# Optimization experiments

Hardware: AMD Instinct MI355X
Metric: run time of the kernel (lower is better)

Reference implementation:

```python
import jax, jax.numpy as jnp
import numpy as np
import math

GROUPS = 32  # min(256 // 4, 32)
EPS = 1e-5

def group_norm(x, w, b):
    B, C, H, W = x.shape
    xg = x.reshape(B, GROUPS, C // GROUPS, H, W)
    mean = jnp.mean(xg, axis=(2, 3, 4), keepdims=True)
    var = jnp.var(xg, axis=(2, 3, 4), keepdims=True)
    xn = ((xg - mean) * jax.lax.rsqrt(var + EPS)).reshape(B, C, H, W)
    return xn * w[None, :, None, None] + b[None, :, None, None]

def nin(x, W, b):
    # 1x1 projection: [B,C,H,W] x [C,D] -> [B,D,H,W]
    return jnp.einsum('bchw,cd->bdhw', x, W) + b[None, :, None, None]

def setup_inputs() -> dict:
    key = jax.random.key(0)
    ks = jax.random.split(key, 5)
    C = 256
    scale = 1.0 / math.sqrt(C)
    return {
        'x': jax.random.normal(ks[0], (4, C, 64, 64), dtype=jnp.float32),
        'gn_w': jnp.ones((C,), jnp.float32),
        'gn_b': jnp.zeros((C,), jnp.float32),
        'Wq': jax.random.normal(ks[1], (C, C), jnp.float32) * scale,
        'bq': jnp.zeros((C,), jnp.float32),
        'Wk': jax.random.normal(ks[2], (C, C), jnp.float32) * scale,
        'bk': jnp.zeros((C,), jnp.float32),
        'Wv': jax.random.normal(ks[3], (C, C), jnp.float32) * scale,
        'bv': jnp.zeros((C,), jnp.float32),
        'Wp': jax.random.normal(ks[4], (C, C), jnp.float32) * scale,
        'bp': jnp.zeros((C,), jnp.float32),
    }

def reference(x, gn_w, gn_b, Wq, bq, Wk, bk, Wv, bv, Wp, bp):
    B, C, H, W = x.shape
    h = group_norm(x, gn_w, gn_b)
    q = nin(h, Wq, bq).reshape(B, C, H * W)
    k = nin(h, Wk, bk).reshape(B, C, H * W)
    v = nin(h, Wv, bv).reshape(B, C, H * W)
    # attention logits: [B, HW, HW]
    w = jnp.einsum('bcn,bcm->bnm', q, k) * (C ** -0.5)
    w = jax.nn.softmax(w, axis=-1)
    h_out = jnp.einsum('bnm,bcm->bcn', w, v).reshape(B, C, H, W)
    h_out = nin(h_out, Wp, bp)
    out = x + h_out
    return out / math.sqrt(2.0)  # skip_rescale=True
```

## Files before the change

kernel.cpp:

```cpp
#include <hip/hip_runtime.h>
#include <math.h>


#define BB 4
#define CCH 256
#define NSP 4096
#define EPSV 1e-5f
#define ATTN_SCALE 0.0625f
#define RSQRT2 0.70710678118654752440f
#define KSPLIT 2
#define TILES_PER_PART 32

typedef __attribute__((ext_vector_type(8))) short bf16x8;
typedef __attribute__((ext_vector_type(4))) float f32x4;

typedef __attribute__((address_space(1))) void gvoid;
typedef __attribute__((address_space(3))) void lvoid;
__device__ __forceinline__ void dma16(const void* g, void* l) {
  __builtin_amdgcn_global_load_lds((gvoid*)g, (lvoid*)l, 16, 0, 0);
}

__device__ __forceinline__ short f2bf(float f) {
  union { float f; unsigned u; } a; a.f = f;
  unsigned r = a.u + 0x7fffu + ((a.u >> 16) & 1u);
  return (short)(r >> 16);
}
__device__ __forceinline__ float bf2f(short s) {
  union { unsigned u; float f; } a;
  a.u = ((unsigned)(unsigned short)s) << 16;
  return a.f;
}
__device__ __forceinline__ unsigned cvt_pk_bf16(float lo, float hi) {
  unsigned r;
  asm("v_cvt_pk_bf16_f32 %0, %1, %2" : "=v"(r) : "v"(lo), "v"(hi));
  return r;
}

__global__ __launch_bounds__(256) void gn_stats(
    const float* __restrict__ x, float* __restrict__ stats) {
  int b = blockIdx.x >> 5;
  int g = blockIdx.x & 31;
  size_t base = ((size_t)b * CCH + (size_t)g * 8) * NSP;
  const float4* xv = (const float4*)(x + base);
  int tid = threadIdx.x;
  float s = 0.f, ss = 0.f;
  for (int i = tid; i < 8192; i += 256) {
    float4 v = xv[i];
    s += (v.x + v.y) + (v.z + v.w);
    ss += (v.x * v.x + v.y * v.y) + (v.z * v.z + v.w * v.w);
  }
#pragma unroll
  for (int off = 32; off > 0; off >>= 1) {
    s += __shfl_down(s, off, 64);
    ss += __shfl_down(ss, off, 64);
  }
  __shared__ float rs[4], rss[4];
  int wv = tid >> 6;
  if ((tid & 63) == 0) { rs[wv] = s; rss[wv] = ss; }
  __syncthreads();
  if (tid == 0) {
    float S = rs[0] + rs[1] + rs[2] + rs[3];
    float SS = rss[0] + rss[1] + rss[2] + rss[3];
    float mean = S * (1.f / 32768.f);
    float var = SS * (1.f / 32768.f) - mean * mean;
    stats[(b * 32 + g) * 2 + 0] = mean;
    stats[(b * 32 + g) * 2 + 1] = rsqrtf(var + EPSV);
  }
}

__global__ __launch_bounds__(256) void prep_w(
    const float* __restrict__ Wq, const float* __restrict__ Wk,
    const float* __restrict__ Wv, const float* __restrict__ Wp,
    short* __restrict__ wts) {
  __shared__ float T[64][65];
  int c0 = blockIdx.x * 64, d0 = blockIdx.y * 64;
  int wz = blockIdx.z;
  const float* W = (wz == 0) ? Wq : (wz == 1) ? Wk : (wz == 2) ? Wv : Wp;
  short* wt = wts + (size_t)wz * CCH * CCH;
  int tid = threadIdx.x;
#pragma unroll
  for (int i = 0; i < 16; ++i) {
    int idx = tid + 256 * i;
    int row = idx >> 6, col = idx & 63;
    T[row][col] = W[(size_t)(c0 + row) * CCH + d0 + col];
  }
  __syncthreads();
#pragma unroll
  for (int i = 0; i < 16; ++i) {
    int idx = tid + 256 * i;
    int dr = idx >> 6, cc = idx & 63;
    wt[(size_t)(d0 + dr) * CCH + c0 + cc] = f2bf(T[cc][dr]);
  }
}

__global__ __launch_bounds__(512) void qkvg_kernel(
    const float* __restrict__ x, const float* __restrict__ stats,
    const float* __restrict__ gw, const float* __restrict__ gb,
    const short* __restrict__ wqt, const short* __restrict__ wkt,
    const short* __restrict__ wvt,
    const float* __restrict__ bq, const float* __restrict__ bk,
    const float* __restrict__ bv,
    short* __restrict__ qo, short* __restrict__ ko, short* __restrict__ vo) {
  __shared__ __align__(16) unsigned char smem[52224];
  float (*Ts)[68] = (float(*)[68])smem;
  float* aco = (float*)(smem + 17408);
  float* bco = aco + 256;
  short* Hs = (short*)(smem + 19456);
  short* Fo = (short*)smem;

  int bx = blockIdx.x;
  int b = bx & 3, n0 = (bx >> 2) * 64;
  int tid = threadIdx.x;
  if (tid < 256) {
    int g = tid >> 3;
    float mean = stats[(b * 32 + g) * 2 + 0];
    float rstd = stats[(b * 32 + g) * 2 + 1];
    float a = gw[tid] * rstd;
    aco[tid] = a;
    bco[tid] = gb[tid] - mean * a;
  }
  __syncthreads();
  const float* xb = x + (size_t)b * CCH * NSP;
  for (int p = 0; p < 4; ++p) {
    int c0 = p * 64;
#pragma unroll
    for (int i = 0; i < 2; ++i) {
      int crow = (tid >> 4) + i * 32;
      int c = c0 + crow;
      float4 v = *(const float4*)&xb[(size_t)c * NSP + n0 + (tid & 15) * 4];
      float a = aco[c], bb = bco[c];
      v.x = v.x * a + bb; v.y = v.y * a + bb;
      v.z = v.z * a + bb; v.w = v.w * a + bb;
      *(float4*)&Ts[crow][(tid & 15) * 4] = v;
    }
    __syncthreads();
    {
      int n = tid >> 3, seg = tid & 7;
      int cb = seg * 8;
      bf16x8 r;
#pragma unroll
      for (int j = 0; j < 8; ++j) r[j] = f2bf(Ts[cb + j][n]);
      int chunk = (c0 + cb) >> 3;
      *(bf16x8*)(Hs + n * 256 + ((chunk ^ (n & 7)) * 8)) = r;
    }
    __syncthreads();
  }
  int w = tid >> 6, lane = tid & 63, quad = lane >> 4, l16 = lane & 15;
  int wr = w & 3, h = w >> 2;
  bf16x8 a_h[8];
  {
    int row = wr * 16 + l16;
#pragma unroll
    for (int kc = 0; kc < 8; ++kc)
      a_h[kc] = *(bf16x8*)(Hs + row * 256 + (((kc * 4 + quad) ^ (row & 7)) * 8));
  }
  __syncthreads();
  for (int op = 0; op < 3; ++op) {
    const short* wt = (op == 0) ? wqt : (op == 1) ? wkt : wvt;
    const float* bias = (op == 0) ? bq : (op == 1) ? bk : bv;
    f32x4 acc[8];
#pragma unroll
    for (int mb = 0; mb < 8; ++mb) acc[mb] = (f32x4){0.f, 0.f, 0.f, 0.f};
#pragma unroll 4
    for (int mb = 0; mb < 8; ++mb) {
      const short* wp = wt + (size_t)((h * 8 + mb) * 16 + l16) * CCH + quad * 8;
#pragma unroll
      for (int kc = 0; kc < 8; ++kc) {
        bf16x8 af = *(const bf16x8*)(wp + kc * 32);
        acc[mb] = __builtin_amdgcn_mfma_f32_16x16x32_bf16(af, a_h[kc], acc[mb], 0, 0, 0);
      }
    }
    int n = n0 + wr * 16 + l16;
    if (op == 2) {
      short* ob = vo + (size_t)b * CCH * NSP;
      int mm = n & 63, m0_ = n & ~63;
      int mb_ = mm >> 4, qq = (mm >> 2) & 3, rr2 = mm & 3;
      int lc = (mb_ & 1) * 4 + qq;
      int jj = (mb_ >> 1) * 4 + rr2;
      int basen = m0_ + jj;
#pragma unroll
      for (int mb = 0; mb < 8; ++mb)
#pragma unroll
        for (int r = 0; r < 4; ++r) {
          int d = (h * 8 + mb) * 16 + quad * 4 + r;
          ob[(size_t)d * NSP + basen + ((lc ^ (d & 7)) << 3)] =
              f2bf(acc[mb][r] + bias[d]);
        }
    } else {
      float sc = (op == 0) ? ATTN_SCALE : 1.f;
      int nl = wr * 16 + l16;
#pragma unroll
      for (int mb = 0; mb < 8; ++mb)
#pragma unroll
        for (int r = 0; r < 4; ++r) {
          int d = (h * 8 + mb) * 16 + quad * 4 + r;
          Fo[nl * 264 + d] = f2bf((acc[mb][r] + bias[d]) * sc);
        }
      __syncthreads();
      short* ob = ((op == 0) ? qo : ko) + (size_t)b * NSP * CCH;
      {
        int row = tid >> 3, seg = tid & 7, r7 = row & 7;
        short* dst = ob + (size_t)(n0 + row) * CCH + seg * 32;
#pragma unroll
        for (int i = 0; i < 4; ++i) {
          int xch = seg * 4 + i;
          int cs = (xch & 24) | ((xch & 7) ^ r7);
          *(bf16x8*)(dst + i * 8) = *(bf16x8*)(Fo + row * 264 + cs * 8);
        }
      }
      __syncthreads();
    }
  }
}

__global__ __launch_bounds__(256, 1) void attn_kernel(
    const short* __restrict__ q, const short* __restrict__ k,
    const short* __restrict__ v, short* __restrict__ po,
    float* __restrict__ pm, float* __restrict__ pl) {
  __shared__ __align__(16) unsigned char smem[131072];
  short* Ks0 = (short*)smem;
  short* Ks1 = (short*)(smem + 32768);
  short* Vs0 = (short*)(smem + 65536);
  short* Vs1 = (short*)(smem + 98304);
  short* Fo  = (short*)smem;

  int bx = blockIdx.x;
  int grp = bx & 7;
  int b = grp & 3;
  int kh = grp >> 2;
  int n0 = ((bx >> 3) & 31) << 7;
  const short* qb = q + (size_t)b * NSP * CCH;
  const short* kb = k + (size_t)b * NSP * CCH;
  const char*  vbB = (const char*)(v + (size_t)b * CCH * NSP);
  int tid = threadIdx.x;
  int w = tid >> 6, lane = tid & 63, quad = lane >> 4, l16 = lane & 15;
  int mbase = kh * TILES_PER_PART * 64;

  bf16x8 a_q[2][8];
#pragma unroll
  for (int p = 0; p < 2; ++p) {
#pragma unroll
    for (int i = 0; i < 8; ++i) {
      int off = tid * 16 + i * 4096;
      dma16((const char*)(qb + (size_t)(n0 + p * 64) * CCH) + off,
            (char*)Ks0 + off);
    }
    __syncthreads();
    if ((w >> 1) == p) {
#pragma unroll
      for (int qh = 0; qh < 2; ++qh) {
        int row = (w & 1) * 32 + qh * 16 + l16;
#pragma unroll
        for (int kc = 0; kc < 8; ++kc)
          a_q[qh][kc] =
              *(bf16x8*)(Ks0 + row * 256 + (((kc * 4 + quad) ^ (row & 7)) * 8));
      }
    }
    __syncthreads();
  }

#pragma unroll
  for (int i = 0; i < 8; ++i) {
    int off = tid * 16 + i * 4096;
    dma16((const char*)(kb + (size_t)mbase * CCH) + off, (char*)Ks0 + off);
    int c = off >> 7, inrow = off & 127;
    dma16(vbB + (size_t)c * (NSP * 2) + (size_t)mbase * 2 + inrow,
          (char*)Vs0 + off);
  }
  __syncthreads();
#pragma unroll
  for (int i = 0; i < 8; ++i) {
    int off = tid * 16 + i * 4096;
    dma16((const char*)(kb + (size_t)(mbase + 64) * CCH) + off,
          (char*)Ks1 + off);
  }
  f32x4 s_prev[4][2];
#pragma unroll
  for (int mb = 0; mb < 4; ++mb)
#pragma unroll
    for (int qh = 0; qh < 2; ++qh) s_prev[mb][qh] = (f32x4){0.f, 0.f, 0.f, 0.f};
  __builtin_amdgcn_s_setprio(1);
#pragma unroll
  for (int kc = 0; kc < 8; ++kc) {
#pragma unroll
    for (int mb = 0; mb < 4; ++mb) {
      int row = mb * 16 + l16;
      bf16x8 kf = *(bf16x8*)(Ks0 + row * 256 + (((kc * 4 + quad) ^ (row & 7)) * 8));
#pragma unroll
      for (int qh = 0; qh < 2; ++qh)
        s_prev[mb][qh] = __builtin_amdgcn_mfma_f32_16x16x32_bf16(
            kf, a_q[qh][kc], s_prev[mb][qh], 0, 0, 0);
    }
  }
  __builtin_amdgcn_s_setprio(0);
  float mx_c[2];
#pragma unroll
  for (int qh = 0; qh < 2; ++qh) {
    float mx = -1e30f;
#pragma unroll
    for (int mb = 0; mb < 4; ++mb)
#pragma unroll
      for (int r = 0; r < 4; ++r) mx = fmaxf(mx, s_prev[mb][qh][r]);
    mx = fmaxf(mx, __shfl_xor(mx, 16));
    mx = fmaxf(mx, __shfl_xor(mx, 32));
    mx_c[qh] = mx;
  }

  f32x4 accO[16][2];
#pragma unroll
  for (int cb = 0; cb < 16; ++cb)
#pragma unroll
    for (int qh = 0; qh < 2; ++qh) accO[cb][qh] = (f32x4){0.f, 0.f, 0.f, 0.f};
  float m_run[2] = {-1e30f, -1e30f}, l_run[2] = {0.f, 0.f};
  int pc0 = quad ^ (l16 & 7);
  int pc1 = (4 + quad) ^ (l16 & 7);

#pragma unroll 1
  for (int t = 0; t < TILES_PER_PART; ++t) {
    __syncthreads();
    short* Kd = (t & 1) ? Ks1 : Ks0;
    short* Kr = (t & 1) ? Ks0 : Ks1;
    short* Vd = (t & 1) ? Vs0 : Vs1;
    short* Vr = (t & 1) ? Vs1 : Vs0;
    if (t + 2 < TILES_PER_PART) {
      const char* kp = (const char*)(kb + (size_t)(mbase + (t + 2) * 64) * CCH);
#pragma unroll
      for (int i = 0; i < 8; ++i) {
        int off = tid * 16 + i * 4096;
        dma16(kp + off, (char*)Kd + off);
      }
    }
    if (t + 1 < TILES_PER_PART) {
      int m0 = mbase + (t + 1) * 64;
#pragma unroll
      for (int i = 0; i < 8; ++i) {
        int off = tid * 16 + i * 4096;
        int c = off >> 7, inrow = off & 127;
        dma16(vbB + (size_t)c * (NSP * 2) + (size_t)m0 * 2 + inrow,
              (char*)Vd + off);
      }
    }
    f32x4 sn[4][2];
#pragma unroll
    for (int mb = 0; mb < 4; ++mb)
#pragma unroll
      for (int qh = 0; qh < 2; ++qh) sn[mb][qh] = (f32x4){0.f, 0.f, 0.f, 0.f};
    if (t + 1 < TILES_PER_PART) {
      __builtin_amdgcn_s_setprio(1);
#pragma unroll
      for (int kc = 0; kc < 8; ++kc) {
#pragma unroll
        for (int mb = 0; mb < 4; ++mb) {
          int row = mb * 16 + l16;
          bf16x8 kf = *(bf16x8*)(Kr + row * 256 + (((kc * 4 + quad) ^ (row & 7)) * 8));
#pragma unroll
          for (int qh = 0; qh < 2; ++qh)
            sn[mb][qh] = __builtin_amdgcn_mfma_f32_16x16x32_bf16(
                kf, a_q[qh][kc], sn[mb][qh], 0, 0, 0);
        }
      }
      __builtin_amdgcn_s_setprio(0);
    }
    bool grow = (mx_c[0] - m_run[0] > 8.f) || (mx_c[1] - m_run[1] > 8.f);
    if (__any(grow)) {
#pragma unroll
      for (int qh = 0; qh < 2; ++qh) {
        float mnew = fmaxf(m_run[qh], mx_c[qh]);
        float alpha = __expf(m_run[qh] - mnew);
#pragma unroll
        for (int cb = 0; cb < 16; ++cb) accO[cb][qh] *= alpha;
        l_run[qh] *= alpha;
        m_run[qh] = mnew;
      }
    }
#pragma unroll
    for (int qh = 0; qh < 2; ++qh) {
      float ls = 0.f;
#pragma unroll
      for (int mb = 0; mb < 4; ++mb)
#pragma unroll
        for (int r = 0; r < 4; ++r) {
          float p = __expf(s_prev[mb][qh][r] - m_run[qh]);
          ls += p;
          s_prev[mb][qh][r] = p;
        }
      ls += __shfl_xor(ls, 16);
      ls += __shfl_xor(ls, 32);
      l_run[qh] += ls;
    }
    union { unsigned u[4]; bf16x8 v; } pw0[2], pw1[2];
#pragma unroll
    for (int qh = 0; qh < 2; ++qh) {
      pw0[qh].u[0] = cvt_pk_bf16(s_prev[0][qh][0], s_prev[0][qh][1]);
      pw0[qh].u[1] = cvt_pk_bf16(s_prev[0][qh][2], s_prev[0][qh][3]);
      pw0[qh].u[2] = cvt_pk_bf16(s_prev[2][qh][0], s_prev[2][qh][1]);
      pw0[qh].u[3] = cvt_pk_bf16(s_prev[2][qh][2], s_prev[2][qh][3]);
      pw1[qh].u[0] = cvt_pk_bf16(s_prev[1][qh][0], s_prev[1][qh][1]);
      pw1[qh].u[1] = cvt_pk_bf16(s_prev[1][qh][2], s_prev[1][qh][3]);
      pw1[qh].u[2] = cvt_pk_bf16(s_prev[3][qh][0], s_prev[3][qh][1]);
      pw1[qh].u[3] = cvt_pk_bf16(s_prev[3][qh][2], s_prev[3][qh][3]);
    }
    __builtin_amdgcn_s_setprio(1);
#pragma unroll
    for (int cb = 0; cb < 16; ++cb) {
      bf16x8 vf = *(bf16x8*)(Vr + (cb * 16 + l16) * 64 + pc0 * 8);
#pragma unroll
      for (int qh = 0; qh < 2; ++qh)
        accO[cb][qh] = __builtin_amdgcn_mfma_f32_16x16x32_bf16(
            vf, pw0[qh].v, accO[cb][qh], 0, 0, 0);
    }
#pragma unroll
    for (int cb = 0; cb < 16; ++cb) {
      bf16x8 vf = *(bf16x8*)(Vr + (cb * 16 + l16) * 64 + pc1 * 8);
#pragma unroll
      for (int qh = 0; qh < 2; ++qh)
        accO[cb][qh] = __builtin_amdgcn_mfma_f32_16x16x32_bf16(
            vf, pw1[qh].v, accO[cb][qh], 0, 0, 0);
    }
    __builtin_amdgcn_s_setprio(0);
    if (t + 1 < TILES_PER_PART) {
#pragma unroll
      for (int qh = 0; qh < 2; ++qh) {
        float mxn = -1e30f;
#pragma unroll
        for (int mb = 0; mb < 4; ++mb)
#pragma unroll
          for (int r = 0; r < 4; ++r) mxn = fmaxf(mxn, sn[mb][qh][r]);
        mxn = fmaxf(mxn, __shfl_xor(mxn, 16));
        mxn = fmaxf(mxn, __shfl_xor(mxn, 32));
        mx_c[qh] = mxn;
      }
    }
#pragma unroll
    for (int mb = 0; mb < 4; ++mb)
#pragma unroll
      for (int qh = 0; qh < 2; ++qh) s_prev[mb][qh] = sn[mb][qh];
  }
  size_t sbase = ((size_t)kh * BB + b) * NSP + n0;
  if (quad == 0) {
#pragma unroll
    for (int qh = 0; qh < 2; ++qh) {
      pm[sbase + w * 32 + qh * 16 + l16] = m_run[qh];
      pl[sbase + w * 32 + qh * 16 + l16] = l_run[qh];
    }
  }
  short* ob = po + ((size_t)kh * BB + b) * NSP * CCH;
#pragma unroll
  for (int p = 0; p < 2; ++p) {
    __syncthreads();
    if ((w >> 1) == p) {
#pragma unroll
      for (int qh = 0; qh < 2; ++qh) {
        int nloc = (w & 1) * 32 + qh * 16 + l16;
        float linv = 1.f / l_run[qh];
#pragma unroll
        for (int cb = 0; cb < 16; ++cb)
#pragma unroll
          for (int r = 0; r < 4; ++r)
            Fo[nloc * 264 + cb * 16 + quad * 4 + r] =
                f2bf(accO[cb][qh][r] * linv);
      }
    }
    __syncthreads();
    int row = tid >> 2, seg = tid & 3;
    short* dst = ob + (size_t)(n0 + p * 64 + row) * CCH + seg * 64;
#pragma unroll
    for (int i = 0; i < 8; ++i)
      *(bf16x8*)(dst + i * 8) = *(bf16x8*)(Fo + row * 264 + seg * 64 + i * 8);
  }
}

__global__ __launch_bounds__(256) void proj_kernel(
    const short* __restrict__ po, const float* __restrict__ pm,
    const float* __restrict__ pl, const short* __restrict__ wpt,
    const float* __restrict__ bp, const float* __restrict__ x,
    float* __restrict__ out) {
  int n0 = blockIdx.x * 64;
  int dh = blockIdx.y * 128;
  int b = blockIdx.z;
  int tid = threadIdx.x;
  int w = tid >> 6, lane = tid & 63, quad = lane >> 4, l16 = lane & 15;
  int n = n0 + w * 16 + l16;

  float wgt[KSPLIT];
  {
    float m[KSPLIT];
    float M = -1e30f;
#pragma unroll
    for (int s = 0; s < KSPLIT; ++s) {
      m[s] = pm[((size_t)s * BB + b) * NSP + n];
      M = fmaxf(M, m[s]);
    }
    float wsum = 0.f;
#pragma unroll
    for (int s = 0; s < KSPLIT; ++s) {
      wgt[s] = __expf(m[s] - M) * pl[((size_t)s * BB + b) * NSP + n];
      wsum += wgt[s];
    }
    float linv = 1.f / wsum;
#pragma unroll
    for (int s = 0; s < KSPLIT; ++s) wgt[s] *= linv;
  }

  f32x4 acc[8];
#pragma unroll
  for (int mb = 0; mb < 8; ++mb) acc[mb] = (f32x4){0.f, 0.f, 0.f, 0.f};

  const short* pob = po + ((size_t)b * NSP + n) * CCH;
#pragma unroll 2
  for (int kc = 0; kc < 8; ++kc) {
    int coff = kc * 32 + quad * 8;
    float e[8];
#pragma unroll
    for (int i = 0; i < 8; ++i) e[i] = 0.f;
#pragma unroll
    for (int s = 0; s < KSPLIT; ++s) {
      bf16x8 f = *(const bf16x8*)(pob + (size_t)s * BB * NSP * CCH + coff);
#pragma unroll
      for (int i = 0; i < 8; ++i) e[i] += wgt[s] * bf2f(f[i]);
    }
    bf16x8 bm;
#pragma unroll
    for (int i = 0; i < 8; ++i) bm[i] = f2bf(e[i]);
#pragma unroll
    for (int mb = 0; mb < 8; ++mb) {
      bf16x8 af = *(const bf16x8*)(wpt + (size_t)(dh + mb * 16 + l16) * CCH + coff);
      acc[mb] = __builtin_amdgcn_mfma_f32_16x16x32_bf16(af, bm, acc[mb], 0, 0, 0);
    }
  }
#pragma unroll
  for (int mb = 0; mb < 8; ++mb) {
#pragma unroll
    for (int r = 0; r < 4; ++r) {
      int d = dh + mb * 16 + quad * 4 + r;
      size_t off = ((size_t)b * CCH + d) * NSP + n;
      out[off] = (acc[mb][r] + bp[d] + x[off]) * RSQRT2;
    }
  }
}

extern "C" void kernel_launch(void* const* d_in, const int* in_sizes, int n_in,
                              void* d_out, int out_size, void* d_ws, size_t ws_size,
                              hipStream_t stream) {
  const float* x  = (const float*)d_in[0];
  const float* gw = (const float*)d_in[1];
  const float* gb = (const float*)d_in[2];
  const float* Wq = (const float*)d_in[3];
  const float* bq = (const float*)d_in[4];
  const float* Wk = (const float*)d_in[5];
  const float* bk = (const float*)d_in[6];
  const float* Wv = (const float*)d_in[7];
  const float* bv = (const float*)d_in[8];
  const float* Wp = (const float*)d_in[9];
  const float* bp = (const float*)d_in[10];
  float* out = (float*)d_out;

  const size_t SZ = (size_t)BB * CCH * NSP;
  short* qb  = (short*)d_ws;
  short* kb  = qb + SZ;
  short* vb  = kb + SZ;
  short* poT = vb + SZ;
  float* pm  = (float*)(poT + (size_t)KSPLIT * SZ);
  float* pl  = pm + (size_t)KSPLIT * BB * NSP;
  float* stats = pl + (size_t)KSPLIT * BB * NSP;
  short* wts = (short*)(stats + BB * 64);
  short* wqt = wts;
  short* wkt = wts + (size_t)CCH * CCH;
  short* wvt = wts + (size_t)2 * CCH * CCH;
  short* wpt = wts + (size_t)3 * CCH * CCH;

  gn_stats<<<dim3(BB * 32), dim3(256), 0, stream>>>(x, stats);
  prep_w<<<dim3(4, 4, 4), dim3(256), 0, stream>>>(Wq, Wk, Wv, Wp, wts);
  qkvg_kernel<<<dim3(256), dim3(512), 0, stream>>>(
      x, stats, gw, gb, wqt, wkt, wvt, bq, bk, bv, qb, kb, vb);
  attn_kernel<<<dim3(BB * 32 * KSPLIT), dim3(256), 0, stream>>>(
      qb, kb, vb, poT, pm, pl);
  proj_kernel<<<dim3(64, 2, BB), dim3(256), 0, stream>>>(
      poT, pm, pl, wpt, bp, x, out);
}
```

Measured before the change: 307.6 us.

## Split attention keys four ways and run two single-buffered blocks per CU

The key dimension is now split into 4 parts of 16 tiles instead of 2 parts of 32, doubling the number of attention blocks. LDS use per block drops from double-buffered 128KB to single-buffered 64KB, and launch bounds now allow 2 blocks per CU. The software pipeline that computed the next tile's QK scores while doing the current PV is replaced by a straightforward per-tile sequence with barriers. The intent is to hide latency across two co-resident blocks rather than inside one block, at the cost of losing the intra-block overlap and doing more partial-result merging downstream.

New measurement: 318.7 us. 1.04x slower.

```diff
diff --git a/kernel.cpp b/kernel.cpp
--- a/kernel.cpp
+++ b/kernel.cpp
@@ -8,8 +8,8 @@
 #define EPSV 1e-5f
 #define ATTN_SCALE 0.0625f
 #define RSQRT2 0.70710678118654752440f
-#define KSPLIT 2
-#define TILES_PER_PART 32
+#define KSPLIT 4
+#define TILES_PER_PART 16
 
 typedef __attribute__((ext_vector_type(8))) short bf16x8;
 typedef __attribute__((ext_vector_type(4))) float f32x4;
@@ -213,22 +213,20 @@
   }
 }
 
-__global__ __launch_bounds__(256, 1) void attn_kernel(
+__global__ __launch_bounds__(256, 2) void attn_kernel(
     const short* __restrict__ q, const short* __restrict__ k,
     const short* __restrict__ v, short* __restrict__ po,
     float* __restrict__ pm, float* __restrict__ pl) {
-  __shared__ __align__(16) unsigned char smem[131072];
-  short* Ks0 = (short*)smem;
-  short* Ks1 = (short*)(smem + 32768);
-  short* Vs0 = (short*)(smem + 65536);
-  short* Vs1 = (short*)(smem + 98304);
-  short* Fo  = (short*)smem;
+  __shared__ __align__(16) unsigned char smem[65536];
+  short* Ks = (short*)smem;
+  short* Vs = (short*)(smem + 32768);
+  short* Fo = (short*)smem;
 
   int bx = blockIdx.x;
-  int grp = bx & 7;
+  int grp = bx & 15;
   int b = grp & 3;
   int kh = grp >> 2;
-  int n0 = ((bx >> 3) & 31) << 7;
+  int n0 = (bx >> 4) << 7;
   const short* qb = q + (size_t)b * NSP * CCH;
   const short* kb = k + (size_t)b * NSP * CCH;
   const char*  vbB = (const char*)(v + (size_t)b * CCH * NSP);
@@ -243,7 +241,7 @@
     for (int i = 0; i < 8; ++i) {
       int off = tid * 16 + i * 4096;
       dma16((const char*)(qb + (size_t)(n0 + p * 64) * CCH) + off,
-            (char*)Ks0 + off);
+            (char*)Ks + off);
     }
     __syncthreads();
     if ((w >> 1) == p) {
@@ -253,7 +251,7 @@
 #pragma unroll
         for (int kc = 0; kc < 8; ++kc)
           a_q[qh][kc] =
-              *(bf16x8*)(Ks0 + row * 256 + (((kc * 4 + quad) ^ (row & 7)) * 8));
+              *(bf16x8*)(Ks + row * 256 + (((kc * 4 + quad) ^ (row & 7)) * 8));
       }
     }
     __syncthreads();
@@ -262,49 +260,12 @@
 #pragma unroll
   for (int i = 0; i < 8; ++i) {
     int off = tid * 16 + i * 4096;
-    dma16((const char*)(kb + (size_t)mbase * CCH) + off, (char*)Ks0 + off);
+    dma16((const char*)(kb + (size_t)mbase * CCH) + off, (char*)Ks + off);
     int c = off >> 7, inrow = off & 127;
     dma16(vbB + (size_t)c * (NSP * 2) + (size_t)mbase * 2 + inrow,
-          (char*)Vs0 + off);
+          (char*)Vs + off);
   }
   __syncthreads();
-#pragma unroll
-  for (int i = 0; i < 8; ++i) {
-    int off = tid * 16 + i * 4096;
-    dma16((const char*)(kb + (size_t)(mbase + 64) * CCH) + off,
-          (char*)Ks1 + off);
-  }
-  f32x4 s_prev[4][2];
-#pragma unroll
-  for (int mb = 0; mb < 4; ++mb)
-#pragma unroll
-    for (int qh = 0; qh < 2; ++qh) s_prev[mb][qh] = (f32x4){0.f, 0.f, 0.f, 0.f};
-  __builtin_amdgcn_s_setprio(1);
-#pragma unroll
-  for (int kc = 0; kc < 8; ++kc) {
-#pragma unroll
-    for (int mb = 0; mb < 4; ++mb) {
-      int row = mb * 16 + l16;
-      bf16x8 kf = *(bf16x8*)(Ks0 + row * 256 + (((kc * 4 + quad) ^ (row & 7)) * 8));
-#pragma unroll
-      for (int qh = 0; qh < 2; ++qh)
-        s_prev[mb][qh] = __builtin_amdgcn_mfma_f32_16x16x32_bf16(
-            kf, a_q[qh][kc], s_prev[mb][qh], 0, 0, 0);
-    }
-  }
-  __builtin_amdgcn_s_setprio(0);
-  float mx_c[2];
-#pragma unroll
-  for (int qh = 0; qh < 2; ++qh) {
-    float mx = -1e30f;
-#pragma unroll
-    for (int mb = 0; mb < 4; ++mb)
-#pragma unroll
-      for (int r = 0; r < 4; ++r) mx = fmaxf(mx, s_prev[mb][qh][r]);
-    mx = fmaxf(mx, __shfl_xor(mx, 16));
-    mx = fmaxf(mx, __shfl_xor(mx, 32));
-    mx_c[qh] = mx;
-  }
 
   f32x4 accO[16][2];
 #pragma unroll
@@ -317,19 +278,104 @@
 
 #pragma unroll 1
   for (int t = 0; t < TILES_PER_PART; ++t) {
-    __syncthreads();
-    short* Kd = (t & 1) ? Ks1 : Ks0;
-    short* Kr = (t & 1) ? Ks0 : Ks1;
-    short* Vd = (t & 1) ? Vs0 : Vs1;
-    short* Vr = (t & 1) ? Vs1 : Vs0;
-    if (t + 2 < TILES_PER_PART) {
-      const char* kp = (const char*)(kb + (size_t)(mbase + (t + 2) * 64) * CCH);
+    f32x4 s[4][2];
+#pragma unroll
+    for (int mb = 0; mb < 4; ++mb)
+#pragma unroll
+      for (int qh = 0; qh < 2; ++qh) s[mb][qh] = (f32x4){0.f, 0.f, 0.f, 0.f};
+    __builtin_amdgcn_s_setprio(1);
+#pragma unroll
+    for (int kc = 0; kc < 8; ++kc) {
+#pragma unroll
+      for (int mb = 0; mb < 4; ++mb) {
+        int row = mb * 16 + l16;
+        bf16x8 kf = *(bf16x8*)(Ks + row * 256 + (((kc * 4 + quad) ^ (row & 7)) * 8));
+#pragma unroll
+        for (int qh = 0; qh < 2; ++qh)
+          s[mb][qh] = __builtin_amdgcn_mfma_f32_16x16x32_bf16(
+              kf, a_q[qh][kc], s[mb][qh], 0, 0, 0);
+      }
+    }
+    __builtin_amdgcn_s_setprio(0);
+    __syncthreads();
+    if (t + 1 < TILES_PER_PART) {
+      const char* kp = (const char*)(kb + (size_t)(mbase + (t + 1) * 64) * CCH);
 #pragma unroll
       for (int i = 0; i < 8; ++i) {
         int off = tid * 16 + i * 4096;
-        dma16(kp + off, (char*)Kd + off);
-      }
-    }
+        dma16(kp + off, (char*)Ks + off);
+      }
+    }
+    float mx[2];
+#pragma unroll
+    for (int qh = 0; qh < 2; ++qh) {
+      float m = -1e30f;
+#pragma unroll
+      for (int mb = 0; mb < 4; ++mb)
+#pragma unroll
+        for (int r = 0; r < 4; ++r) m = fmaxf(m, s[mb][qh][r]);
+      m = fmaxf(m, __shfl_xor(m, 16));
+      m = fmaxf(m, __shfl_xor(m, 32));
+      mx[qh] = m;
+    }
+    bool grow = (mx[0] - m_run[0] > 8.f) || (mx[1] - m_run[1] > 8.f);
+    if (__any(grow)) {
+#pragma unroll
+      for (int qh = 0; qh < 2; ++qh) {
+        float mnew = fmaxf(m_run[qh], mx[qh]);
+        float alpha = __expf(m_run[qh] - mnew);
+#pragma unroll
+        for (int cb = 0; cb < 16; ++cb) accO[cb][qh] *= alpha;
+        l_run[qh] *= alpha;
+        m_run[qh] = mnew;
+      }
+    }
+#pragma unroll
+    for (int qh = 0; qh < 2; ++qh) {
+      float ls = 0.f;
+#pragma unroll
+      for (int mb = 0; mb < 4; ++mb)
+#pragma unroll
+        for (int r = 0; r < 4; ++r) {
+          float p = __expf(s[mb][qh][r] - m_run[qh]);
+          ls += p;
+          s[mb][qh][r] = p;
+        }
+      ls += __shfl_xor(ls, 16);
+      ls += __shfl_xor(ls, 32);
+      l_run[qh] += ls;
+    }
+    union { unsigned u[4]; bf16x8 v; } pw0[2], pw1[2];
+#pragma unroll
+    for (int qh = 0; qh < 2; ++qh) {
+      pw0[qh].u[0] = cvt_pk_bf16(s[0][qh][0], s[0][qh][1]);
+      pw0[qh].u[1] = cvt_pk_bf16(s[0][qh][2], s[0][qh][3]);
+      pw0[qh].u[2] = cvt_pk_bf16(s[2][qh][0], s[2][qh][1]);
+      pw0[qh].u[3] = cvt_pk_bf16(s[2][qh][2], s[2][qh][3]);
+      pw1[qh].u[0] = cvt_pk_bf16(s[1][qh][0], s[1][qh][1]);
+      pw1[qh].u[1] = cvt_pk_bf16(s[1][qh][2], s[1][qh][3]);
+      pw1[qh].u[2] = cvt_pk_bf16(s[3][qh][0], s[3][qh][1]);
+      pw1[qh].u[3] = cvt_pk_bf16(s[3][qh][2], s[3][qh][3]);
+    }
+    __builtin_amdgcn_s_setprio(1);
+#pragma unroll
+    for (int cb = 0; cb < 16; ++cb) {
+      bf16x8 vf = *(bf16x8*)(Vs + (cb * 16 + l16) * 64 + pc0 * 8);
+#pragma unroll
+      for (int qh = 0; qh < 2; ++qh)
+        accO[cb][qh] = __builtin_amdgcn_mfma_f32_16x16x32_bf16(
+            vf, pw0[qh].v, accO[cb][qh], 0, 0, 0);
+    }
+#pragma unroll
+    for (int cb = 0; cb < 16; ++cb) {
+      bf16x8 vf = *(bf16x8*)(Vs + (cb * 16 + l16) * 64 + pc1 * 8);
+#pragma unroll
+      for (int qh = 0; qh < 2; ++qh)
+        accO[cb][qh] = __builtin_amdgcn_mfma_f32_16x16x32_bf16(
+            vf, pw1[qh].v, accO[cb][qh], 0, 0, 0);
+    }
+    __builtin_amdgcn_s_setprio(0);
+    __syncthreads();
     if (t + 1 < TILES_PER_PART) {
       int m0 = mbase + (t + 1) * 64;
 #pragma unroll
@@ -337,111 +383,16 @@
         int off = tid * 16 + i * 4096;
         int c = off >> 7, inrow = off & 127;
         dma16(vbB + (size_t)c * (NSP * 2) + (size_t)m0 * 2 + inrow,
-              (char*)Vd + off);
-      }
-    }
-    f32x4 sn[4][2];
-#pragma unroll
-    for (int mb = 0; mb < 4; ++mb)
-#pragma unroll
-      for (int qh = 0; qh < 2; ++qh) sn[mb][qh] = (f32x4){0.f, 0.f, 0.f, 0.f};
-    if (t + 1 < TILES_PER_PART) {
-      __builtin_amdgcn_s_setprio(1);
-#pragma unroll
-      for (int kc = 0; kc < 8; ++kc) {
-#pragma unroll
-        for (int mb = 0; mb < 4; ++mb) {
-          int row = mb * 16 + l16;
-          bf16x8 kf = *(bf16x8*)(Kr + row * 256 + (((kc * 4 + quad) ^ (row & 7)) * 8));
-#pragma unroll
-          for (int qh = 0; qh < 2; ++qh)
-            sn[mb][qh] = __builtin_amdgcn_mfma_f32_16x16x32_bf16(
-                kf, a_q[qh][kc], sn[mb][qh], 0, 0, 0);
-        }
-      }
-      __builtin_amdgcn_s_setprio(0);
-    }
-    bool grow = (mx_c[0] - m_run[0] > 8.f) || (mx_c[1] - m_run[1] > 8.f);
-    if (__any(grow)) {
-#pragma unroll
-      for (int qh = 0; qh < 2; ++qh) {
-        float mnew = fmaxf(m_run[qh], mx_c[qh]);
-        float alpha = __expf(m_run[qh] - mnew);
-#pragma unroll
-        for (int cb = 0; cb < 16; ++cb) accO[cb][qh] *= alpha;
-        l_run[qh] *= alpha;
-        m_run[qh] = mnew;
-      }
-    }
-#pragma unroll
-    for (int qh = 0; qh < 2; ++qh) {
-      float ls = 0.f;
-#pragma unroll
-      for (int mb = 0; mb < 4; ++mb)
-#pragma unroll
-        for (int r = 0; r < 4; ++r) {
-          float p = __expf(s_prev[mb][qh][r] - m_run[qh]);
-          ls += p;
-          s_prev[mb][qh][r] = p;
-        }
-      ls += __shfl_xor(ls, 16);
-      ls += __shfl_xor(ls, 32);
-      l_run[qh] += ls;
-    }
-    union { unsigned u[4]; bf16x8 v; } pw0[2], pw1[2];
-#pragma unroll
-    for (int qh = 0; qh < 2; ++qh) {
-      pw0[qh].u[0] = cvt_pk_bf16(s_prev[0][qh][0], s_prev[0][qh][1]);
-      pw0[qh].u[1] = cvt_pk_bf16(s_prev[0][qh][2], s_prev[0][qh][3]);
-      pw0[qh].u[2] = cvt_pk_bf16(s_prev[2][qh][0], s_prev[2][qh][1]);
-      pw0[qh].u[3] = cvt_pk_bf16(s_prev[2][qh][2], s_prev[2][qh][3]);
-      pw1[qh].u[0] = cvt_pk_bf16(s_prev[1][qh][0], s_prev[1][qh][1]);
-      pw1[qh].u[1] = cvt_pk_bf16(s_prev[1][qh][2], s_prev[1][qh][3]);
-      pw1[qh].u[2] = cvt_pk_bf16(s_prev[3][qh][0], s_prev[3][qh][1]);
-      pw1[qh].u[3] = cvt_pk_bf16(s_prev[3][qh][2], s_prev[3][qh][3]);
-    }
-    __builtin_amdgcn_s_setprio(1);
-#pragma unroll
-    for (int cb = 0; cb < 16; ++cb) {
-      bf16x8 vf = *(bf16x8*)(Vr + (cb * 16 + l16) * 64 + pc0 * 8);
-#pragma unroll
-      for (int qh = 0; qh < 2; ++qh)
-        accO[cb][qh] = __builtin_amdgcn_mfma_f32_16x16x32_bf16(
-            vf, pw0[qh].v, accO[cb][qh], 0, 0, 0);
-    }
-#pragma unroll
-    for (int cb = 0; cb < 16; ++cb) {
-      bf16x8 vf = *(bf16x8*)(Vr + (cb * 16 + l16) * 64 + pc1 * 8);
-#pragma unroll
-      for (int qh = 0; qh < 2; ++qh)
-        accO[cb][qh] = __builtin_amdgcn_mfma_f32_16x16x32_bf16(
-            vf, pw1[qh].v, accO[cb][qh], 0, 0, 0);
-    }
-    __builtin_amdgcn_s_setprio(0);
-    if (t + 1 < TILES_PER_PART) {
-#pragma unroll
-      for (int qh = 0; qh < 2; ++qh) {
-        float mxn = -1e30f;
-#pragma unroll
-        for (int mb = 0; mb < 4; ++mb)
-#pragma unroll
-          for (int r = 0; r < 4; ++r) mxn = fmaxf(mxn, sn[mb][qh][r]);
-        mxn = fmaxf(mxn, __shfl_xor(mxn, 16));
-        mxn = fmaxf(mxn, __shfl_xor(mxn, 32));
-        mx_c[qh] = mxn;
-      }
-    }
-#pragma unroll
-    for (int mb = 0; mb < 4; ++mb)
-#pragma unroll
-      for (int qh = 0; qh < 2; ++qh) s_prev[mb][qh] = sn[mb][qh];
+              (char*)Vs + off);
+      }
+    }
   }
   size_t sbase = ((size_t)kh * BB + b) * NSP + n0;
   if (quad == 0) {
 #pragma unroll
     for (int qh = 0; qh < 2; ++qh) {
-      pm[sbase + w * 32 + qh * 16 + l16] = m_run[qh];
-      pl[sbase + w * 32 + qh * 16 + l16] = l_run[qh];
+      pm[sbase + (w & 1) * 32 + (w >> 1) * 64 + qh * 16 + l16] = m_run[qh];
+      pl[sbase + (w & 1) * 32 + (w >> 1) * 64 + qh * 16 + l16] = l_run[qh];
     }
   }
   short* ob = po + ((size_t)kh * BB + b) * NSP * CCH;
```
